# Kernel tuning notes

Hardware: AMD Instinct MI355X
Metric: run time of the kernel (lower is better)

## Reference

```python
import jax, jax.numpy as jnp
import numpy as np

D_MODEL = 1024
NHEAD = 16
HEAD_DIM = D_MODEL // NHEAD
D_FF = 4096
EPS = 1e-5


def _linear(x, w, b):
    # torch Linear: y = x @ W^T + b, W is [out, in]
    return x @ w.T + b


def _layernorm(x, g, b):
    mu = jnp.mean(x, axis=-1, keepdims=True)
    var = jnp.var(x, axis=-1, keepdims=True)
    return (x - mu) * jax.lax.rsqrt(var + EPS) * g + b


def setup_inputs() -> dict:
    key = jax.random.key(0)
    ks = jax.random.split(key, 16)
    s = 0.02
    inp = {
        'x': jax.random.normal(ks[0], (2048, D_MODEL), jnp.float32),
        'q_in_w': s * jax.random.normal(ks[1], (D_MODEL, D_MODEL), jnp.float32),
        'q_in_b': jnp.zeros((D_MODEL,), jnp.float32),
        'k_in_w': s * jax.random.normal(ks[2], (D_MODEL, D_MODEL), jnp.float32),
        'k_in_b': jnp.zeros((D_MODEL,), jnp.float32),
        'v_in_w': s * jax.random.normal(ks[3], (D_MODEL, D_MODEL), jnp.float32),
        'v_in_b': jnp.zeros((D_MODEL,), jnp.float32),
        'out_w': s * jax.random.normal(ks[4], (D_MODEL, D_MODEL), jnp.float32),
        'out_b': jnp.zeros((D_MODEL,), jnp.float32),
        'ffn1_w': s * jax.random.normal(ks[5], (D_FF, D_MODEL), jnp.float32),
        'ffn1_b': jnp.zeros((D_FF,), jnp.float32),
        'ffn2_w': s * jax.random.normal(ks[6], (D_MODEL, D_FF), jnp.float32),
        'ffn2_b': jnp.zeros((D_MODEL,), jnp.float32),
        'n1_g': jnp.ones((D_MODEL,), jnp.float32),
        'n1_b': jnp.zeros((D_MODEL,), jnp.float32),
        'n2_g': jnp.ones((D_MODEL,), jnp.float32),
        'n2_b': jnp.zeros((D_MODEL,), jnp.float32),
        'q_out_w': s * jax.random.normal(ks[7], (D_MODEL, D_MODEL), jnp.float32),
        'q_out_b': jnp.zeros((D_MODEL,), jnp.float32),
        'k_out_w': s * jax.random.normal(ks[8], (D_MODEL, D_MODEL), jnp.float32),
        'k_out_b': jnp.zeros((D_MODEL,), jnp.float32),
        'v_out_w': s * jax.random.normal(ks[9], (D_MODEL, D_MODEL), jnp.float32),
        'v_out_b': jnp.zeros((D_MODEL,), jnp.float32),
        'seq_length': 2048,
    }
    return inp


def reference(x, q_in_w, q_in_b, k_in_w, k_in_b, v_in_w, v_in_b,
              out_w, out_b, ffn1_w, ffn1_b, ffn2_w, ffn2_b,
              n1_g, n1_b, n2_g, n2_b,
              q_out_w, q_out_b, k_out_w, k_out_b, v_out_w, v_out_b,
              seq_length):
    S = seq_length
    # --- is_first: batched in-projections (replaces per-token loop + cat) ---
    q_buf = _linear(x, q_in_w, q_in_b)   # [S, D]
    k_buf = _linear(x, k_in_w, k_in_b)
    v_buf = _linear(x, v_in_w, v_in_b)
    prev_layer_input = x

    # --- multi-head attention (non-causal, no mask) ---
    q = q_buf.reshape(S, NHEAD, HEAD_DIM).transpose(1, 0, 2)  # [H, S, Dh]
    k = k_buf.reshape(S, NHEAD, HEAD_DIM).transpose(1, 0, 2)
    v = v_buf.reshape(S, NHEAD, HEAD_DIM).transpose(1, 0, 2)
    scale = 1.0 / np.sqrt(HEAD_DIM).astype(np.float32)
    scores = jnp.einsum('hqd,hkd->hqk', q, k) * scale        # [H, S, S]
    attn = jax.nn.softmax(scores, axis=-1)
    ctx = jnp.einsum('hqk,hkd->hqd', attn, v)                # [H, S, Dh]
    attn_output = ctx.transpose(1, 0, 2).reshape(S, D_MODEL)  # [S, D]

    # --- post-norm residual blocks (batched over tokens) ---
    h = _linear(attn_output, out_w, out_b)
    h = _layernorm(prev_layer_input + h, n1_g, n1_b)
    ff = _linear(jax.nn.relu(_linear(h, ffn1_w, ffn1_b)), ffn2_w, ffn2_b)
    y = _layernorm(h + ff, n2_g, n2_b)                        # [S, D]

    # --- not is_last: out-projections for the next layer ---
    q_next = _linear(y, q_out_w, q_out_b)
    k_next = _linear(y, k_out_w, k_out_b)
    v_next = _linear(y, v_out_w, v_out_b)
    return (q_next, k_next, v_next, y)
```

## Files before the change

kernel.cpp:

```cpp
#include <hip/hip_runtime.h>
#include <math.h>

#define SEQ   2048
#define DM    1024
#define NH    16
#define DH    64
#define DFF   4096
#define KVSPLIT 4

typedef __bf16 bf16;
using bf16x8 = __attribute__((ext_vector_type(8))) __bf16;
using f32x4  = __attribute__((ext_vector_type(4))) float;

__device__ __forceinline__ unsigned short f2bfu(float f) {
    unsigned int u = __float_as_uint(f);
    u += 0x7FFF + ((u >> 16) & 1);
    return (unsigned short)(u >> 16);
}
__device__ __forceinline__ bf16 f2bf(float f) {
    unsigned short s = f2bfu(f);
    return __builtin_bit_cast(bf16, s);
}

__device__ __forceinline__ void gll16(const bf16* g, bf16* lds_base) {
    __builtin_amdgcn_global_load_lds(
        (const __attribute__((address_space(1))) unsigned int*)g,
        (__attribute__((address_space(3))) unsigned int*)lds_base, 16, 0, 0);
}

__global__ __launch_bounds__(256) void conv_k(const float* __restrict__ src,
                                              bf16* __restrict__ dst, int n) {
    int i = (blockIdx.x * 256 + threadIdx.x) * 4;
    if (i >= n) return;
    float4 v = *(const float4*)(src + i);
    ushort4 o;
    o.x = f2bfu(v.x); o.y = f2bfu(v.y); o.z = f2bfu(v.z); o.w = f2bfu(v.w);
    *(ushort4*)((unsigned short*)dst + i) = o;
}

struct ConvSeg  { const float* src; bf16* dst; int n; };
struct ConvSegs { ConvSeg s[6]; };

__global__ __launch_bounds__(256) void conv_multi_k(ConvSegs cs) {
    ConvSeg sg = cs.s[blockIdx.y];
    int i = (blockIdx.x * 256 + threadIdx.x) * 4;
    if (i >= sg.n) return;
    float4 v = *(const float4*)(sg.src + i);
    ushort4 o;
    o.x = f2bfu(v.x); o.y = f2bfu(v.y); o.z = f2bfu(v.z); o.w = f2bfu(v.w);
    *(ushort4*)((unsigned short*)sg.dst + i) = o;
}

struct GemmPtrs {
    const bf16* W[3];
    const float* bias[3];
    float* out32[3];
    bf16*  out16[3];
};

template<int BM, int BN>
__global__ __launch_bounds__(256) void gemm_bf16_k(
    const bf16* __restrict__ A, GemmPtrs p, int N, int K, int relu)
{
    constexpr int TM = BM / 32;
    constexpr int TN = BN / 32;
    __shared__ bf16 As[BM][32];
    __shared__ bf16 Ws[BN][32];

    const int t    = threadIdx.x;
    const int lane = t & 63;
    const int wave = t >> 6;
    const int quad = lane >> 4;
    const int l15  = lane & 15;
    const int wm   = (wave >> 1) * (BM / 2);
    const int wn   = (wave & 1) * (BN / 2);
    const int m0   = blockIdx.y * BM;
    const int n0   = blockIdx.x * BN;
    const bf16* __restrict__ W = p.W[blockIdx.z];

    f32x4 acc[TM][TN];
    #pragma unroll
    for (int i = 0; i < TM; ++i)
        #pragma unroll
        for (int j = 0; j < TN; ++j)
            acc[i][j] = f32x4{0.f, 0.f, 0.f, 0.f};

    for (int k0 = 0; k0 < K; k0 += 32) {
        #pragma unroll
        for (int s = 0; s < BM / 64; ++s) {
            int base = s * 256 + wave * 64;
            int idx  = base + lane;
            gll16(A + (long)(m0 + (idx >> 2)) * K + k0 + (idx & 3) * 8,
                  &As[0][0] + (long)base * 8);
        }
        #pragma unroll
        for (int s = 0; s < BN / 64; ++s) {
            int base = s * 256 + wave * 64;
            int idx  = base + lane;
            gll16(W + (long)(n0 + (idx >> 2)) * K + k0 + (idx & 3) * 8,
                  &Ws[0][0] + (long)base * 8);
        }
        __syncthreads();

        bf16x8 a[TM], b[TN];
        #pragma unroll
        for (int i = 0; i < TM; ++i)
            a[i] = *(const bf16x8*)&As[wm + i * 16 + l15][quad * 8];
        #pragma unroll
        for (int j = 0; j < TN; ++j)
            b[j] = *(const bf16x8*)&Ws[wn + j * 16 + l15][quad * 8];
        #pragma unroll
        for (int i = 0; i < TM; ++i)
            #pragma unroll
            for (int j = 0; j < TN; ++j)
                acc[i][j] = __builtin_amdgcn_mfma_f32_16x16x32_bf16(
                    a[i], b[j], acc[i][j], 0, 0, 0);
        __syncthreads();
    }

    float* o32 = p.out32[blockIdx.z];
    bf16*  o16 = p.out16[blockIdx.z];
    const float* bias = p.bias[blockIdx.z];
    #pragma unroll
    for (int j = 0; j < TN; ++j) {
        int n = n0 + wn + j * 16 + l15;
        float bv = bias[n];
        #pragma unroll
        for (int i = 0; i < TM; ++i) {
            #pragma unroll
            for (int r = 0; r < 4; ++r) {
                int m = m0 + wm + i * 16 + quad * 4 + r;
                float v = acc[i][j][r] + bv;
                if (relu) v = fmaxf(v, 0.f);
                if (o32) o32[(long)m * N + n] = v;
                if (o16) o16[(long)m * N + n] = f2bf(v);
            }
        }
    }
}

template<int BM, int BN, int KS>
__global__ __launch_bounds__(256) void gemm_splitk_k(
    const bf16* __restrict__ A, const bf16* __restrict__ W,
    float* __restrict__ part, int N, int K)
{
    constexpr int TM = BM / 32;
    constexpr int TN = BN / 32;
    __shared__ bf16 As[BM][32];
    __shared__ bf16 Ws[BN][32];

    const int t    = threadIdx.x;
    const int lane = t & 63;
    const int wave = t >> 6;
    const int quad = lane >> 4;
    const int l15  = lane & 15;
    const int wm   = (wave >> 1) * (BM / 2);
    const int wn   = (wave & 1) * (BN / 2);
    const int m0   = blockIdx.y * BM;
    const int n0   = blockIdx.x * BN;
    const int Kp   = K / KS;
    const int klo  = blockIdx.z * Kp;
    const long MN  = (long)gridDim.y * BM * N;

    f32x4 acc[TM][TN];
    #pragma unroll
    for (int i = 0; i < TM; ++i)
        #pragma unroll
        for (int j = 0; j < TN; ++j)
            acc[i][j] = f32x4{0.f, 0.f, 0.f, 0.f};

    for (int k0 = klo; k0 < klo + Kp; k0 += 32) {
        #pragma unroll
        for (int s = 0; s < BM / 64; ++s) {
            int base = s * 256 + wave * 64;
            int idx  = base + lane;
            gll16(A + (long)(m0 + (idx >> 2)) * K + k0 + (idx & 3) * 8,
                  &As[0][0] + (long)base * 8);
        }
        #pragma unroll
        for (int s = 0; s < BN / 64; ++s) {
            int base = s * 256 + wave * 64;
            int idx  = base + lane;
            gll16(W + (long)(n0 + (idx >> 2)) * K + k0 + (idx & 3) * 8,
                  &Ws[0][0] + (long)base * 8);
        }
        __syncthreads();

        bf16x8 a[TM], b[TN];
        #pragma unroll
        for (int i = 0; i < TM; ++i)
            a[i] = *(const bf16x8*)&As[wm + i * 16 + l15][quad * 8];
        #pragma unroll
        for (int j = 0; j < TN; ++j)
            b[j] = *(const bf16x8*)&Ws[wn + j * 16 + l15][quad * 8];
        #pragma unroll
        for (int i = 0; i < TM; ++i)
            #pragma unroll
            for (int j = 0; j < TN; ++j)
                acc[i][j] = __builtin_amdgcn_mfma_f32_16x16x32_bf16(
                    a[i], b[j], acc[i][j], 0, 0, 0);
        __syncthreads();
    }

    float* o = part + (long)blockIdx.z * MN;
    #pragma unroll
    for (int j = 0; j < TN; ++j) {
        int n = n0 + wn + j * 16 + l15;
        #pragma unroll
        for (int i = 0; i < TM; ++i)
            #pragma unroll
            for (int r = 0; r < 4; ++r) {
                int m = m0 + wm + i * 16 + quad * 4 + r;
                o[(long)m * N + n] = acc[i][j][r];
            }
    }
}

__global__ __launch_bounds__(256) void attn_mfma_k(
    const bf16* __restrict__ Q, const bf16* __restrict__ Kg,
    const bf16* __restrict__ Vg, bf16* __restrict__ Opart,
    float* __restrict__ lpart)
{
    __shared__ bf16 Kb[64][64];
    __shared__ bf16 Vt[64][72];

    const int t    = threadIdx.x;
    const int lane = t & 63;
    const int wave = t >> 6;
    const int quad = lane >> 4;
    const int l15  = lane & 15;
    const int h    = blockIdx.y;
    const int q0   = blockIdx.x * 64;
    const int spl  = blockIdx.z;
    const int cb   = h * DH;
    const long SD  = (long)SEQ * DM;

    const int qrow = q0 + wave * 16 + l15;
    bf16x8 bQ[2];
    #pragma unroll
    for (int kh = 0; kh < 2; ++kh)
        bQ[kh] = *(const bf16x8*)(Q + (long)qrow * DM + cb + kh * 32 + quad * 8);

    f32x4 o_acc[4];
    #pragma unroll
    for (int dt = 0; dt < 4; ++dt) o_acc[dt] = f32x4{0.f, 0.f, 0.f, 0.f};
    float lsum = 0.f;

    const float SCL = 0.18033688f;
    const int kv_lo = spl * (SEQ / KVSPLIT);
    const int kv_hi = kv_lo + SEQ / KVSPLIT;

    for (int kv0 = kv_lo; kv0 < kv_hi; kv0 += 64) {
        __syncthreads();
        #pragma unroll
        for (int s = 0; s < 2; ++s) {
            int idx = s * 256 + t;
            int row = idx >> 3;
            int dg  = idx & 7;
            gll16(Kg + (long)(kv0 + row) * DM + cb + ((dg ^ (row & 7)) * 8),
                  &Kb[0][0] + (s * 256 + wave * 64) * 8);
        }
        #pragma unroll
        for (int s = 0; s < 2; ++s) {
            int idx = t + s * 256;
            int key = idx >> 3;
            int dg  = idx & 7;
            bf16x8 vv = *(const bf16x8*)(Vg + (long)(kv0 + key) * DM + cb + dg * 8);
            int vk  = (key & 0x20) | ((key & 0x0f) << 1) | ((key & 0x10) >> 4);
            int swz = vk ^ (dg * 8);
            #pragma unroll
            for (int j = 0; j < 8; ++j) Vt[dg * 8 + j][swz] = vv[j];
        }
        __syncthreads();

        float p[16];
        #pragma unroll
        for (int kt = 0; kt < 4; ++kt) {
            int krow = kt * 16 + l15;
            bf16x8 a0 = *(const bf16x8*)&Kb[krow][(quad ^ (l15 & 7)) * 8];
            bf16x8 a1 = *(const bf16x8*)&Kb[krow][((4 + quad) ^ (l15 & 7)) * 8];
            f32x4 sv = f32x4{0.f, 0.f, 0.f, 0.f};
            sv = __builtin_amdgcn_mfma_f32_16x16x32_bf16(a0, bQ[0], sv, 0, 0, 0);
            sv = __builtin_amdgcn_mfma_f32_16x16x32_bf16(a1, bQ[1], sv, 0, 0, 0);
            #pragma unroll
            for (int r = 0; r < 4; ++r) p[kt * 4 + r] = exp2f(sv[r] * SCL);
        }

        bf16x8 aP[2];
        #pragma unroll
        for (int c = 0; c < 2; ++c)
            #pragma unroll
            for (int j = 0; j < 8; ++j) {
                float pv = p[(2 * c + (j & 1)) * 4 + (j >> 1)];
                lsum += pv;
                aP[c][j] = f2bf(pv);
            }

        #pragma unroll
        for (int dt = 0; dt < 4; ++dt) {
            int d   = dt * 16 + l15;
            int dgr = d >> 3;
            bf16x8 v0 = *(const bf16x8*)&Vt[d][(quad ^ dgr) * 8];
            bf16x8 v1 = *(const bf16x8*)&Vt[d][((4 + quad) ^ dgr) * 8];
            o_acc[dt] = __builtin_amdgcn_mfma_f32_16x16x32_bf16(aP[0], v0, o_acc[dt], 0, 0, 0);
            o_acc[dt] = __builtin_amdgcn_mfma_f32_16x16x32_bf16(aP[1], v1, o_acc[dt], 0, 0, 0);
        }
    }

    #pragma unroll
    for (int r = 0; r < 4; ++r) {
        int row = q0 + wave * 16 + quad * 4 + r;
        #pragma unroll
        for (int dt = 0; dt < 4; ++dt)
            Opart[(long)spl * SD + (long)row * DM + cb + dt * 16 + l15] =
                f2bf(o_acc[dt][r]);
    }
    lsum += __shfl_xor(lsum, 16);
    lsum += __shfl_xor(lsum, 32);
    if (quad == 0)
        lpart[((long)spl * NH + h) * SEQ + qrow] = lsum;
}

__global__ __launch_bounds__(256) void attn_reduce_k(
    const bf16* __restrict__ Opart, const float* __restrict__ lpart,
    bf16* __restrict__ O)
{
    const long SD = (long)SEQ * DM;
    long i = ((long)blockIdx.x * 256 + threadIdx.x) * 8;
    int row = (int)(i / DM);
    int h   = (int)((i % DM) / DH);

    float l = 0.f;
    #pragma unroll
    for (int k = 0; k < KVSPLIT; ++k)
        l += lpart[((long)k * NH + h) * SEQ + row];
    float inv = 1.f / l;

    float acc[8] = {};
    #pragma unroll
    for (int k = 0; k < KVSPLIT; ++k) {
        bf16x8 v = *(const bf16x8*)(Opart + (long)k * SD + i);
        #pragma unroll
        for (int j = 0; j < 8; ++j) acc[j] += (float)v[j];
    }
    bf16x8 o;
    #pragma unroll
    for (int j = 0; j < 8; ++j) o[j] = f2bf(acc[j] * inv);
    *(bf16x8*)(O + i) = o;
}

template<int NS>
__global__ __launch_bounds__(256) void ln_red_k(
    const float* __restrict__ part, const float* __restrict__ bias,
    const float* __restrict__ res, const float* __restrict__ g,
    const float* __restrict__ b, float* __restrict__ out32,
    bf16* __restrict__ out16)
{
    const long SD = (long)SEQ * DM;
    const int row = blockIdx.x;
    const int t   = threadIdx.x;
    const long off = (long)row * DM + (t << 2);

    float4 v = *(const float4*)(res + off);
    float4 bv0 = *(const float4*)(bias + (t << 2));
    v.x += bv0.x; v.y += bv0.y; v.z += bv0.z; v.w += bv0.w;
    #pragma unroll
    for (int z = 0; z < NS; ++z) {
        float4 pz = *(const float4*)(part + z * SD + off);
        v.x += pz.x; v.y += pz.y; v.z += pz.z; v.w += pz.w;
    }

    float s1 = v.x + v.y + v.z + v.w;
    float s2 = v.x * v.x + v.y * v.y + v.z * v.z + v.w * v.w;
    #pragma unroll
    for (int off2 = 32; off2 > 0; off2 >>= 1) {
        s1 += __shfl_xor(s1, off2);
        s2 += __shfl_xor(s2, off2);
    }
    __shared__ float red[8];
    int wid = t >> 6, lid = t & 63;
    if (lid == 0) { red[wid] = s1; red[4 + wid] = s2; }
    __syncthreads();
    s1 = red[0] + red[1] + red[2] + red[3];
    s2 = red[4] + red[5] + red[6] + red[7];

    float mu   = s1 * (1.f / DM);
    float var  = s2 * (1.f / DM) - mu * mu;
    float rstd = rsqrtf(var + 1e-5f);

    float4 gv = *(const float4*)(g + (t << 2));
    float4 bv = *(const float4*)(b + (t << 2));
    float4 ov;
    ov.x = (v.x - mu) * rstd * gv.x + bv.x;
    ov.y = (v.y - mu) * rstd * gv.y + bv.y;
    ov.z = (v.z - mu) * rstd * gv.z + bv.z;
    ov.w = (v.w - mu) * rstd * gv.w + bv.w;
    if (out32) *(float4*)(out32 + off) = ov;
    if (out16) {
        ushort4 o;
        o.x = f2bfu(ov.x); o.y = f2bfu(ov.y); o.z = f2bfu(ov.z); o.w = f2bfu(ov.w);
        *(ushort4*)((unsigned short*)out16 + off) = o;
    }
}

extern "C" void kernel_launch(void* const* d_in, const int* in_sizes, int n_in,
                              void* d_out, int out_size, void* d_ws, size_t ws_size,
                              hipStream_t stream)
{
    const float* x       = (const float*)d_in[0];
    const float* q_in_w  = (const float*)d_in[1];
    const float* q_in_b  = (const float*)d_in[2];
    const float* k_in_w  = (const float*)d_in[3];
    const float* k_in_b  = (const float*)d_in[4];
    const float* v_in_w  = (const float*)d_in[5];
    const float* v_in_b  = (const float*)d_in[6];
    const float* out_w   = (const float*)d_in[7];
    const float* out_b   = (const float*)d_in[8];
    const float* ffn1_w  = (const float*)d_in[9];
    const float* ffn1_b  = (const float*)d_in[10];
    const float* ffn2_w  = (const float*)d_in[11];
    const float* ffn2_b  = (const float*)d_in[12];
    const float* n1_g    = (const float*)d_in[13];
    const float* n1_b    = (const float*)d_in[14];
    const float* n2_g    = (const float*)d_in[15];
    const float* n2_b    = (const float*)d_in[16];
    const float* q_out_w = (const float*)d_in[17];
    const float* q_out_b = (const float*)d_in[18];
    const float* k_out_w = (const float*)d_in[19];
    const float* k_out_b = (const float*)d_in[20];
    const float* v_out_w = (const float*)d_in[21];
    const float* v_out_b = (const float*)d_in[22];

    float* out = (float*)d_out;
    const long SD = (long)SEQ * DM;
    const long MB = 1024 * 1024;

    char* w = (char*)d_ws;
    bf16*  xbf   = (bf16*)(w);
    float* lpart = (float*)(w);
    bf16*  qb    = (bf16*)(w + 4  * MB);
    bf16*  kb    = (bf16*)(w + 8  * MB);
    bf16*  vb    = (bf16*)(w + 12 * MB);
    bf16*  atnb  = (bf16*)(w + 16 * MB);
    float* h32   = (float*)(w);
    bf16*  h16   = (bf16*)(w + 8  * MB);
    float* P2    = (float*)(w + 8  * MB);
    bf16*  Opart = (bf16*)(w + 20 * MB);
    float* P1    = (float*)(w + 20 * MB);
    bf16*  f1    = (bf16*)(w + 24 * MB);
    bf16*  wqi   = (bf16*)(w + 32 * MB);
    bf16*  wki   = (bf16*)(w + 34 * MB);
    bf16*  wvi   = (bf16*)(w + 36 * MB);
    bf16*  wo    = (bf16*)(w + 38 * MB);
    bf16*  wf1   = (bf16*)(w + 40 * MB);
    bf16*  wf2   = (bf16*)(w + 40 * MB);
    bf16*  wqo   = (bf16*)(w + 24 * MB);
    bf16*  wko   = (bf16*)(w + 26 * MB);
    bf16*  wvo   = (bf16*)(w + 28 * MB);
    bf16*  ybf   = (bf16*)(w + 30 * MB);
    float* y32   = out + 3 * SD;

    dim3 blk(256);
    const int DD = DM * DM;

    {
        ConvSegs cs;
        cs.s[0] = {x,      xbf, (int)SD};
        cs.s[1] = {q_in_w, wqi, DD};
        cs.s[2] = {k_in_w, wki, DD};
        cs.s[3] = {v_in_w, wvi, DD};
        cs.s[4] = {out_w,  wo,  DD};
        cs.s[5] = {ffn1_w, wf1, DM * DFF};
        conv_multi_k<<<dim3(DM * DFF / 1024, 6), blk, 0, stream>>>(cs);
    }

    {
        GemmPtrs p{};
        p.W[0] = wqi; p.W[1] = wki; p.W[2] = wvi;
        p.bias[0] = q_in_b; p.bias[1] = k_in_b; p.bias[2] = v_in_b;
        p.out16[0] = qb; p.out16[1] = kb; p.out16[2] = vb;
        gemm_bf16_k<128, 128><<<dim3(DM / 128, SEQ / 128, 3), blk, 0, stream>>>(
            xbf, p, DM, DM, 0);
    }

    attn_mfma_k<<<dim3(SEQ / 64, NH, KVSPLIT), blk, 0, stream>>>(
        qb, kb, vb, Opart, lpart);
    attn_reduce_k<<<dim3((int)(SD / 2048)), blk, 0, stream>>>(Opart, lpart, atnb);

    gemm_splitk_k<64, 128, 2><<<dim3(DM / 128, SEQ / 64, 2), blk, 0, stream>>>(
        atnb, wo, P1, DM, DM);

    ln_red_k<2><<<SEQ, blk, 0, stream>>>(P1, out_b, x, n1_g, n1_b, h32, h16);

    {
        GemmPtrs p{};
        p.W[0] = wf1; p.bias[0] = ffn1_b; p.out16[0] = f1;
        gemm_bf16_k<128, 128><<<dim3(DFF / 128, SEQ / 128, 1), blk, 0, stream>>>(
            h16, p, DFF, DM, 1);
    }

    conv_k<<<dim3(DM * DFF / 1024), blk, 0, stream>>>(ffn2_w, wf2, DM * DFF);

    gemm_splitk_k<128, 128, 2><<<dim3(DM / 128, SEQ / 128, 2), blk, 0, stream>>>(
        f1, wf2, P2, DM, DFF);

    {
        ConvSegs cs;
        cs.s[0] = {q_out_w, wqo, DD};
        cs.s[1] = {k_out_w, wko, DD};
        cs.s[2] = {v_out_w, wvo, DD};
        cs.s[3] = cs.s[0]; cs.s[4] = cs.s[0]; cs.s[5] = cs.s[0];
        conv_multi_k<<<dim3(DD / 1024, 3), blk, 0, stream>>>(cs);
    }

    ln_red_k<2><<<SEQ, blk, 0, stream>>>(P2, ffn2_b, h32, n2_g, n2_b, y32, ybf);

    {
        GemmPtrs p{};
        p.W[0] = wqo; p.W[1] = wko; p.W[2] = wvo;
        p.bias[0] = q_out_b; p.bias[1] = k_out_b; p.bias[2] = v_out_b;
        p.out32[0] = out; p.out32[1] = out + SD; p.out32[2] = out + 2 * SD;
        gemm_bf16_k<128, 128><<<dim3(DM / 128, SEQ / 128, 3), blk, 0, stream>>>(
            ybf, p, DM, DM, 0);
    }
}
```

Baseline: 374.0 us.

## Deepen GEMM K-tile to 64 with XOR-swizzled LDS and smaller N tiles

The bf16 GEMM and split-K GEMM kernels now take a BK template parameter. They stage 64-wide K tiles into LDS using an XOR swizzle on 16-byte chunks so that fragment reads avoid bank conflicts, and issue two MFMA k-steps per barrier pair. Launch shapes change to 128x64 tiles for the plain GEMMs and 64x128 for the FFN2 split-K, raising block counts for better CU occupancy. This halves the number of sync points per K, at the cost of more LDS per block and, for the narrower tiles, lower operand reuse.

```diff
diff --git a/kernel.cpp b/kernel.cpp
--- a/kernel.cpp
+++ b/kernel.cpp
@@ -58,14 +58,16 @@
     bf16*  out16[3];
 };
 
-template<int BM, int BN>
+template<int BM, int BN, int BK>
 __global__ __launch_bounds__(256) void gemm_bf16_k(
     const bf16* __restrict__ A, GemmPtrs p, int N, int K, int relu)
 {
     constexpr int TM = BM / 32;
     constexpr int TN = BN / 32;
-    __shared__ bf16 As[BM][32];
-    __shared__ bf16 Ws[BN][32];
+    constexpr int KK = BK / 32;
+    constexpr int CH = BK / 8;
+    __shared__ bf16 As[BM][BK];
+    __shared__ bf16 Ws[BN][BK];
 
     const int t    = threadIdx.x;
     const int lane = t & 63;
@@ -76,6 +78,7 @@
     const int wn   = (wave & 1) * (BN / 2);
     const int m0   = blockIdx.y * BM;
     const int n0   = blockIdx.x * BN;
+    const int xm   = l15 & (CH - 1);
     const bf16* __restrict__ W = p.W[blockIdx.z];
 
     f32x4 acc[TM][TN];
@@ -85,36 +88,48 @@
         for (int j = 0; j < TN; ++j)
             acc[i][j] = f32x4{0.f, 0.f, 0.f, 0.f};
 
-    for (int k0 = 0; k0 < K; k0 += 32) {
-        #pragma unroll
-        for (int s = 0; s < BM / 64; ++s) {
+    for (int k0 = 0; k0 < K; k0 += BK) {
+        #pragma unroll
+        for (int s = 0; s < BM * BK / 2048; ++s) {
             int base = s * 256 + wave * 64;
             int idx  = base + lane;
-            gll16(A + (long)(m0 + (idx >> 2)) * K + k0 + (idx & 3) * 8,
+            int row  = idx / CH;
+            int c    = idx % CH;
+            gll16(A + (long)(m0 + row) * K + k0 + ((c ^ (row & (CH - 1))) * 8),
                   &As[0][0] + (long)base * 8);
         }
         #pragma unroll
-        for (int s = 0; s < BN / 64; ++s) {
+        for (int s = 0; s < BN * BK / 2048; ++s) {
             int base = s * 256 + wave * 64;
             int idx  = base + lane;
-            gll16(W + (long)(n0 + (idx >> 2)) * K + k0 + (idx & 3) * 8,
+            int row  = idx / CH;
+            int c    = idx % CH;
+            gll16(W + (long)(n0 + row) * K + k0 + ((c ^ (row & (CH - 1))) * 8),
                   &Ws[0][0] + (long)base * 8);
         }
         __syncthreads();
 
-        bf16x8 a[TM], b[TN];
+        bf16x8 a[TM][KK], b[TN][KK];
         #pragma unroll
         for (int i = 0; i < TM; ++i)
-            a[i] = *(const bf16x8*)&As[wm + i * 16 + l15][quad * 8];
+            #pragma unroll
+            for (int kk = 0; kk < KK; ++kk)
+                a[i][kk] = *(const bf16x8*)
+                    &As[wm + i * 16 + l15][((kk * 4 + quad) ^ xm) * 8];
         #pragma unroll
         for (int j = 0; j < TN; ++j)
-            b[j] = *(const bf16x8*)&Ws[wn + j * 16 + l15][quad * 8];
-        #pragma unroll
-        for (int i = 0; i < TM; ++i)
-            #pragma unroll
-            for (int j = 0; j < TN; ++j)
-                acc[i][j] = __builtin_amdgcn_mfma_f32_16x16x32_bf16(
-                    a[i], b[j], acc[i][j], 0, 0, 0);
+            #pragma unroll
+            for (int kk = 0; kk < KK; ++kk)
+                b[j][kk] = *(const bf16x8*)
+                    &Ws[wn + j * 16 + l15][((kk * 4 + quad) ^ xm) * 8];
+        #pragma unroll
+        for (int kk = 0; kk < KK; ++kk)
+            #pragma unroll
+            for (int i = 0; i < TM; ++i)
+                #pragma unroll
+                for (int j = 0; j < TN; ++j)
+                    acc[i][j] = __builtin_amdgcn_mfma_f32_16x16x32_bf16(
+                        a[i][kk], b[j][kk], acc[i][j], 0, 0, 0);
         __syncthreads();
     }
 
@@ -139,15 +154,17 @@
     }
 }
 
-template<int BM, int BN, int KS>
+template<int BM, int BN, int BK, int KS>
 __global__ __launch_bounds__(256) void gemm_splitk_k(
     const bf16* __restrict__ A, const bf16* __restrict__ W,
     float* __restrict__ part, int N, int K)
 {
     constexpr int TM = BM / 32;
     constexpr int TN = BN / 32;
-    __shared__ bf16 As[BM][32];
-    __shared__ bf16 Ws[BN][32];
+    constexpr int KK = BK / 32;
+    constexpr int CH = BK / 8;
+    __shared__ bf16 As[BM][BK];
+    __shared__ bf16 Ws[BN][BK];
 
     const int t    = threadIdx.x;
     const int lane = t & 63;
@@ -158,6 +175,7 @@
     const int wn   = (wave & 1) * (BN / 2);
     const int m0   = blockIdx.y * BM;
     const int n0   = blockIdx.x * BN;
+    const int xm   = l15 & (CH - 1);
     const int Kp   = K / KS;
     const int klo  = blockIdx.z * Kp;
     const long MN  = (long)gridDim.y * BM * N;
@@ -169,36 +187,48 @@
         for (int j = 0; j < TN; ++j)
             acc[i][j] = f32x4{0.f, 0.f, 0.f, 0.f};
 
-    for (int k0 = klo; k0 < klo + Kp; k0 += 32) {
-        #pragma unroll
-        for (int s = 0; s < BM / 64; ++s) {
+    for (int k0 = klo; k0 < klo + Kp; k0 += BK) {
+        #pragma unroll
+        for (int s = 0; s < BM * BK / 2048; ++s) {
             int base = s * 256 + wave * 64;
             int idx  = base + lane;
-            gll16(A + (long)(m0 + (idx >> 2)) * K + k0 + (idx & 3) * 8,
+            int row  = idx / CH;
+            int c    = idx % CH;
+            gll16(A + (long)(m0 + row) * K + k0 + ((c ^ (row & (CH - 1))) * 8),
                   &As[0][0] + (long)base * 8);
         }
         #pragma unroll
-        for (int s = 0; s < BN / 64; ++s) {
+        for (int s = 0; s < BN * BK / 2048; ++s) {
             int base = s * 256 + wave * 64;
             int idx  = base + lane;
-            gll16(W + (long)(n0 + (idx >> 2)) * K + k0 + (idx & 3) * 8,
+            int row  = idx / CH;
+            int c    = idx % CH;
+            gll16(W + (long)(n0 + row) * K + k0 + ((c ^ (row & (CH - 1))) * 8),
                   &Ws[0][0] + (long)base * 8);
         }
         __syncthreads();
 
-        bf16x8 a[TM], b[TN];
+        bf16x8 a[TM][KK], b[TN][KK];
         #pragma unroll
         for (int i = 0; i < TM; ++i)
-            a[i] = *(const bf16x8*)&As[wm + i * 16 + l15][quad * 8];
+            #pragma unroll
+            for (int kk = 0; kk < KK; ++kk)
+                a[i][kk] = *(const bf16x8*)
+                    &As[wm + i * 16 + l15][((kk * 4 + quad) ^ xm) * 8];
         #pragma unroll
         for (int j = 0; j < TN; ++j)
-            b[j] = *(const bf16x8*)&Ws[wn + j * 16 + l15][quad * 8];
-        #pragma unroll
-        for (int i = 0; i < TM; ++i)
-            #pragma unroll
-            for (int j = 0; j < TN; ++j)
-                acc[i][j] = __builtin_amdgcn_mfma_f32_16x16x32_bf16(
-                    a[i], b[j], acc[i][j], 0, 0, 0);
+            #pragma unroll
+            for (int kk = 0; kk < KK; ++kk)
+                b[j][kk] = *(const bf16x8*)
+                    &Ws[wn + j * 16 + l15][((kk * 4 + quad) ^ xm) * 8];
+        #pragma unroll
+        for (int kk = 0; kk < KK; ++kk)
+            #pragma unroll
+            for (int i = 0; i < TM; ++i)
+                #pragma unroll
+                for (int j = 0; j < TN; ++j)
+                    acc[i][j] = __builtin_amdgcn_mfma_f32_16x16x32_bf16(
+                        a[i][kk], b[j][kk], acc[i][j], 0, 0, 0);
         __syncthreads();
     }
 
@@ -479,7 +509,7 @@
         p.W[0] = wqi; p.W[1] = wki; p.W[2] = wvi;
         p.bias[0] = q_in_b; p.bias[1] = k_in_b; p.bias[2] = v_in_b;
         p.out16[0] = qb; p.out16[1] = kb; p.out16[2] = vb;
-        gemm_bf16_k<128, 128><<<dim3(DM / 128, SEQ / 128, 3), blk, 0, stream>>>(
+        gemm_bf16_k<128, 64, 64><<<dim3(DM / 64, SEQ / 128, 3), blk, 0, stream>>>(
             xbf, p, DM, DM, 0);
     }
 
@@ -487,7 +517,7 @@
         qb, kb, vb, Opart, lpart);
     attn_reduce_k<<<dim3((int)(SD / 2048)), blk, 0, stream>>>(Opart, lpart, atnb);
 
-    gemm_splitk_k<64, 128, 2><<<dim3(DM / 128, SEQ / 64, 2), blk, 0, stream>>>(
+    gemm_splitk_k<64, 128, 64, 2><<<dim3(DM / 128, SEQ / 64, 2), blk, 0, stream>>>(
         atnb, wo, P1, DM, DM);
 
     ln_red_k<2><<<SEQ, blk, 0, stream>>>(P1, out_b, x, n1_g, n1_b, h32, h16);
@@ -495,13 +525,13 @@
     {
         GemmPtrs p{};
         p.W[0] = wf1; p.bias[0] = ffn1_b; p.out16[0] = f1;
-        gemm_bf16_k<128, 128><<<dim3(DFF / 128, SEQ / 128, 1), blk, 0, stream>>>(
+        gemm_bf16_k<128, 64, 64><<<dim3(DFF / 64, SEQ / 128, 1), blk, 0, stream>>>(
             h16, p, DFF, DM, 1);
     }
 
     conv_k<<<dim3(DM * DFF / 1024), blk, 0, stream>>>(ffn2_w, wf2, DM * DFF);
 
-    gemm_splitk_k<128, 128, 2><<<dim3(DM / 128, SEQ / 128, 2), blk, 0, stream>>>(
+    gemm_splitk_k<64, 128, 64, 2><<<dim3(DM / 128, SEQ / 64, 2), blk, 0, stream>>>(
         f1, wf2, P2, DM, DFF);
 
     {
@@ -520,7 +550,7 @@
         p.W[0] = wqo; p.W[1] = wko; p.W[2] = wvo;
         p.bias[0] = q_out_b; p.bias[1] = k_out_b; p.bias[2] = v_out_b;
         p.out32[0] = out; p.out32[1] = out + SD; p.out32[2] = out + 2 * SD;
-        gemm_bf16_k<128, 128><<<dim3(DM / 128, SEQ / 128, 3), blk, 0, stream>>>(
+        gemm_bf16_k<128, 64, 64><<<dim3(DM / 64, SEQ / 128, 3), blk, 0, stream>>>(
             ybf, p, DM, DM, 0);
     }
 }
```

Measured after the change: 327.3 us. 12.5% less time.
